# Kernel tuning notes

Hardware: AMD Instinct MI355X
Metric: run time of the kernel (lower is better)

Reference implementation:

```python
import jax, jax.numpy as jnp
import numpy as np

B, L, D, H, E, K = 16, 197, 768, 12, 8, 2
HID = 4 * D
HD = D // H
SCALE = HD ** -0.5
EPS = 1e-5


def _layernorm(x, g, b):
    m = jnp.mean(x, axis=-1, keepdims=True)
    v = jnp.mean((x - m) ** 2, axis=-1, keepdims=True)
    return (x - m) * jax.lax.rsqrt(v + EPS) * g + b


def setup_inputs() -> dict:
    key = jax.random.key(0)
    ks = jax.random.split(key, 8)
    s = 0.02
    return {
        "x": jax.random.normal(ks[0], (B, L, D), jnp.float32),
        "ln1_g": jnp.ones((D,), jnp.float32),
        "ln1_b": jnp.zeros((D,), jnp.float32),
        "qkv_w": jax.random.normal(ks[1], (D, 3 * D), jnp.float32) * s,
        "qkv_b": jnp.zeros((3 * D,), jnp.float32),
        "proj_w": jax.random.normal(ks[2], (D, D), jnp.float32) * s,
        "proj_b": jnp.zeros((D,), jnp.float32),
        "ln2_g": jnp.ones((D,), jnp.float32),
        "ln2_b": jnp.zeros((D,), jnp.float32),
        "w_gate": jax.random.normal(ks[3], (D, E), jnp.float32) * s,
        "w1": jax.random.normal(ks[4], (E, D, HID), jnp.float32) * s,
        "b1": jnp.zeros((E, HID), jnp.float32),
        "w2": jax.random.normal(ks[5], (E, HID, D), jnp.float32) * s,
        "b2": jnp.zeros((E, D), jnp.float32),
    }


def reference(x, ln1_g, ln1_b, qkv_w, qkv_b, proj_w, proj_b,
              ln2_g, ln2_b, w_gate, w1, b1, w2, b2):
    # --- attention branch: x = x + attn(norm1(x)) ---
    h = _layernorm(x, ln1_g, ln1_b)
    qkv = (h @ qkv_w + qkv_b).reshape(B, L, 3, H, HD)
    q, k, v = [qkv[:, :, i].transpose(0, 2, 1, 3) for i in range(3)]  # [B,H,L,HD]
    attn = jax.nn.softmax(jnp.einsum('bhqd,bhkd->bhqk', q, k) * SCALE, axis=-1)
    o = jnp.einsum('bhqk,bhkd->bhqd', attn, v).transpose(0, 2, 1, 3).reshape(B, L, D)
    x = x + o @ proj_w + proj_b

    # --- MoE FFN branch on norm2(x), tokens flattened ---
    flat = _layernorm(x, ln2_g, ln2_b).reshape(-1, D)  # [T, D], T = B*L
    T = flat.shape[0]
    # noisy top-k gating, eval path (no noise): top-(k+1) logits, softmax over top-k
    logits = flat @ w_gate                              # [T, E]
    top_vals, top_idx = jax.lax.top_k(logits, K + 1)
    probs = jax.nn.softmax(top_vals[:, :K], axis=-1)    # [T, K]
    gates = jnp.zeros((T, E), flat.dtype).at[
        jnp.arange(T)[:, None], top_idx[:, :K]].set(probs)  # sparse gate matrix

    # dense equivalent of SparseDispatcher dispatch -> expert MLP -> combine:
    # output[t] = sum_e gates[t,e] * (gelu(flat @ w1[e] + b1[e]) @ w2[e] + b2[e])
    hid = jax.nn.gelu(jnp.einsum('td,edf->tef', flat, w1) + b1, approximate=False)
    y = jnp.einsum('te,tef,efd->td', gates, hid, w2) + gates @ b2
    return x + y.reshape(B, L, D)
```

## Files before the change

kernel.cpp:

```cpp
#include <hip/hip_runtime.h>
#include <math.h>
#include <stdint.h>

typedef unsigned short u16;
typedef unsigned int u32;
typedef float floatx4 __attribute__((ext_vector_type(4)));
typedef __bf16 bf16x8 __attribute__((ext_vector_type(8)));

#define T_TOK 3152
#define SEQ 197
#define NH 12
#define LISTN 7424
#define MOE_MT 58

__device__ __forceinline__ float bf2f(u16 u) { return __uint_as_float(((u32)u) << 16); }
__device__ __forceinline__ u16 f2bf(float f) {
    u32 u = __float_as_uint(f);
    u += 0x7FFFu + ((u >> 16) & 1u);
    return (u16)(u >> 16);
}
__device__ __forceinline__ float wred_sum(float v) {
#pragma unroll
    for (int off = 32; off; off >>= 1) v += __shfl_xor(v, off);
    return v;
}
__device__ __forceinline__ int wred_sum_i(int v) {
#pragma unroll
    for (int off = 32; off; off >>= 1) v += __shfl_xor(v, off);
    return v;
}

__device__ __forceinline__ float gelu_fast(float v) {
    float x = fabsf(v) * 0.70710678118654752f;
    float t = __builtin_amdgcn_rcpf(fmaf(0.3275911f, x, 1.0f));
    float p = t * fmaf(t, fmaf(t, fmaf(t, fmaf(t, 1.061405429f, -1.453152027f),
                                       1.421413741f), -0.284496736f), 0.254829592f);
    float er = fmaf(-p, __expf(-x * x), 1.0f);
    er = copysignf(er, v);
    return 0.5f * v * (1.0f + er);
}

#define GLB_AS(p) ((const __attribute__((address_space(1))) void*)(uintptr_t)(p))
#define LDS_AS(p) ((__attribute__((address_space(3))) void*)(uintptr_t)(p))
__device__ __forceinline__ void gl_lds16(const u16* g, u16* l) {
    __builtin_amdgcn_global_load_lds(GLB_AS(g), LDS_AS(l), 16, 0, 0);
}

__device__ __forceinline__ void transp_tile(const float* __restrict__ in,
        u16* __restrict__ oh, u16* __restrict__ ol, int R, int C,
        int rt, int ct, int z, bool split, float (*Lt)[68]) {
    int r0 = rt * 64, c0 = ct * 64;
    size_t zo = (size_t)z * R * C;
    int tid = threadIdx.x;
    int rr = tid >> 2, cs = (tid & 3) * 16;
    const float* src = in + zo + (size_t)(r0 + rr) * C + c0 + cs;
#pragma unroll
    for (int i = 0; i < 4; i++) *(float4*)&Lt[rr][cs + i * 4] = *(const float4*)(src + i * 4);
    __syncthreads();
    int cw = tid >> 2, rs = (tid & 3) * 16;
    u16 hv[16], lv[16];
#pragma unroll
    for (int j2 = 0; j2 < 16; j2++) {
        float v = Lt[rs + j2][cw];
        u16 hb = f2bf(v);
        hv[j2] = hb;
        if (split) lv[j2] = f2bf(v - bf2f(hb));
    }
    u16* dst = oh + zo + (size_t)(c0 + cw) * R + r0 + rs;
    *(uint4*)dst = *(const uint4*)&hv[0];
    *(uint4*)(dst + 8) = *(const uint4*)&hv[8];
    if (split) {
        u16* dstl = ol + zo + (size_t)(c0 + cw) * R + r0 + rs;
        *(uint4*)dstl = *(const uint4*)&lv[0];
        *(uint4*)(dstl + 8) = *(const uint4*)&lv[8];
    }
}

#define PREP_QKVT 432
#define PREP_PROJT 144
#define PREP_W1T 4608
#define PREP_W2T 4608
#define PREP_TOTAL (PREP_QKVT + PREP_PROJT + PREP_W1T + PREP_W2T + 1)

__global__ __launch_bounds__(256) void prep_kernel(
        const float* __restrict__ qkv_w, u16* __restrict__ qkvt_h, u16* __restrict__ qkvt_l,
        const float* __restrict__ proj_w, u16* __restrict__ projt_h, u16* __restrict__ projt_l,
        const float* __restrict__ w1, u16* __restrict__ w1t,
        const float* __restrict__ w2, u16* __restrict__ w2t,
        const float* __restrict__ wg, float* __restrict__ wgT) {
    __shared__ float Lt[64][68];
    int bid = blockIdx.x;
    if (bid < PREP_QKVT) {
        transp_tile(qkv_w, qkvt_h, qkvt_l, 768, 2304, bid % 12, bid / 12, 0, true, Lt);
    } else if (bid < PREP_QKVT + PREP_PROJT) {
        int lb = bid - PREP_QKVT;
        transp_tile(proj_w, projt_h, projt_l, 768, 768, lb % 12, lb / 12, 0, true, Lt);
    } else if (bid < PREP_QKVT + PREP_PROJT + PREP_W1T) {
        int lb = bid - (PREP_QKVT + PREP_PROJT);
        int z = lb / (12 * 48), rem = lb % (12 * 48);
        transp_tile(w1, w1t, nullptr, 768, 3072, rem % 12, rem / 12, z, false, Lt);
    } else if (bid < PREP_QKVT + PREP_PROJT + PREP_W1T + PREP_W2T) {
        int lb = bid - (PREP_QKVT + PREP_PROJT + PREP_W1T);
        int z = lb / (48 * 12), rem = lb % (48 * 12);
        transp_tile(w2, w2t, nullptr, 3072, 768, rem % 48, rem / 48, z, false, Lt);
    } else {
        for (int i = threadIdx.x; i < 768 * 8; i += 256) {
            int d2 = i >> 3, e = i & 7;
            wgT[e * 768 + d2] = wg[i];
        }
    }
}

__global__ __launch_bounds__(256) void ln1_kernel(const float* __restrict__ x,
        const float* __restrict__ g, const float* __restrict__ b,
        u16* __restrict__ h_hi, u16* __restrict__ h_lo) {
    int t = blockIdx.x, tid = threadIdx.x;
    int w = tid >> 6, lane = tid & 63;
    float v[3];
#pragma unroll
    for (int i = 0; i < 3; i++) v[i] = x[(size_t)t * 768 + tid + i * 256];
    float s = v[0] + v[1] + v[2];
    float q = v[0] * v[0] + v[1] * v[1] + v[2] * v[2];
    s = wred_sum(s); q = wred_sum(q);
    __shared__ float red[8];
    if (lane == 0) { red[w] = s; red[4 + w] = q; }
    __syncthreads();
    float st = red[0] + red[1] + red[2] + red[3];
    float qt = red[4] + red[5] + red[6] + red[7];
    float mean = st * (1.f / 768.f);
    float var = qt * (1.f / 768.f) - mean * mean;
    float rs = rsqrtf(var + 1e-5f);
#pragma unroll
    for (int i = 0; i < 3; i++) {
        int d = tid + i * 256;
        float hv = (v[i] - mean) * rs * g[d] + b[d];
        u16 hi = f2bf(hv);
        h_hi[(size_t)t * 768 + d] = hi;
        h_lo[(size_t)t * 768 + d] = f2bf(hv - bf2f(hi));
    }
}

template <int MODE>
__global__ __launch_bounds__(256) void gemm128(const u16* __restrict__ Ah,
        const u16* __restrict__ Al, const u16* __restrict__ Bh, const u16* __restrict__ Bl,
        const float* __restrict__ bias, void* __restrict__ Cv, void* __restrict__ Cv2,
        const float* __restrict__ resid,
        const int* __restrict__ list, const int* __restrict__ asg, int M, int N, int K) {
    constexpr bool SPLIT = (MODE <= 1);
    constexpr int GX = (MODE <= 1) ? 25 : MOE_MT;
    constexpr int GY = (MODE == 0) ? 18 : (MODE == 2) ? 24 : 6;
    constexpr int GZ = (MODE == 3) ? 2 : 1;
    constexpr int G  = GX * GY * GZ;
    constexpr int NT = GY * GZ;
    constexpr int Q8 = G >> 3, R8 = G & 7;

    int d = blockIdx.x + GX * (blockIdx.y + GY * blockIdx.z);
    int j = d & 7, s = d >> 3;
    int v = (j < R8) ? (j * (Q8 + 1) + s) : (R8 * (Q8 + 1) + (j - R8) * Q8 + s);
    int mt = v / NT, nzr = v - mt * NT;
    int yt = nzr % GY, zt = nzr / GY;
    int m0 = mt * 128, n0 = yt * 128;

    const u16* Bph = Bh;
    const float* bp = bias;
    const u16* Bpl = Bl;
    if (MODE >= 2) {
        if (m0 >= asg[8]) return;
        int e = 0;
        while (m0 >= asg[e + 1]) ++e;
        Bph = Bh + (size_t)e * N * K;
        bp = bias + (size_t)e * N;
    }
    int kbeg = 0, kend = K;
    if (MODE == 3) { int kh = K >> 1; kbeg = zt * kh; kend = kbeg + kh; }

    __shared__ __align__(16) u16 SM[SPLIT ? 32768 : 24576];
    u16* Ash = SM;
    u16* Bsh = SM + (SPLIT ? 8192 : 12288);
    u16* Asl = SM + 16384;
    u16* Bsl = SM + 24576;

    int tid = threadIdx.x;
    int w = tid >> 6, lane = tid & 63, l15 = lane & 15, quad = lane >> 4;
    int wm = (w & 1) * 64, wn = (w >> 1) * 64;
    int lr = lane >> 2;
    int lc = ((lane & 3) ^ ((lane >> 3) & 3)) * 8;

    const u16* ga[2]; const u16* gal[2];
    const u16* gb[2]; const u16* gbl[2];
    int ldro[2];
#pragma unroll
    for (int it = 0; it < 2; it++) {
        int arow = m0 + it * 64 + w * 16 + lr;
        if (MODE == 2) {
            int entry = list[arow];
            ga[it] = Ah + (size_t)(entry >= 0 ? (entry >> 1) : 0) * K + lc;
        } else if (MODE == 3) {
            ga[it] = Ah + (size_t)arow * K + lc;
        } else {
            int rc = min(arow, M - 1);
            ga[it] = Ah + (size_t)rc * K + lc;
            gal[it] = Al + (size_t)rc * K + lc;
        }
        int brow = n0 + it * 64 + w * 16 + lr;
        gb[it] = Bph + (size_t)brow * K + lc;
        if (SPLIT) gbl[it] = Bpl + (size_t)brow * K + lc;
        ldro[it] = (it * 64 + w * 16) * 32;
    }

    int ra[4], rb[4];
#pragma unroll
    for (int i = 0; i < 4; i++) {
        int r1 = wm + i * 16 + l15;
        ra[i] = r1 * 32 + (quad ^ ((r1 >> 1) & 3)) * 8;
        int r2 = wn + i * 16 + l15;
        rb[i] = r2 * 32 + (quad ^ ((r2 >> 1) & 3)) * 8;
    }

    floatx4 acc[4][4];
#pragma unroll
    for (int mi = 0; mi < 4; mi++)
#pragma unroll
        for (int ni = 0; ni < 4; ni++) acc[mi][ni] = (floatx4){0.f, 0.f, 0.f, 0.f};

    auto stage = [&](int buf, int k0) {
        int bo = buf * 4096;
#pragma unroll
        for (int it = 0; it < 2; it++) {
            gl_lds16(ga[it] + k0, &Ash[bo + ldro[it]]);
            gl_lds16(gb[it] + k0, &Bsh[bo + ldro[it]]);
            if constexpr (SPLIT) {
                gl_lds16(gal[it] + k0, &Asl[bo + ldro[it]]);
                gl_lds16(gbl[it] + k0, &Bsl[bo + ldro[it]]);
            }
        }
    };
    auto compute = [&](int buf) {
        int bo = buf * 4096;
        bf16x8 afh[4], bfh[4], afl[4], bfl[4];
#pragma unroll
        for (int i = 0; i < 4; i++) {
            afh[i] = *(const bf16x8*)&Ash[bo + ra[i]];
            bfh[i] = *(const bf16x8*)&Bsh[bo + rb[i]];
            if constexpr (SPLIT) {
                afl[i] = *(const bf16x8*)&Asl[bo + ra[i]];
                bfl[i] = *(const bf16x8*)&Bsl[bo + rb[i]];
            }
        }
        __builtin_amdgcn_s_setprio(1);
#pragma unroll
        for (int mi = 0; mi < 4; mi++)
#pragma unroll
            for (int ni = 0; ni < 4; ni++) {
                if constexpr (SPLIT) {
                    acc[mi][ni] = __builtin_amdgcn_mfma_f32_16x16x32_bf16(afl[mi], bfh[ni], acc[mi][ni], 0, 0, 0);
                    acc[mi][ni] = __builtin_amdgcn_mfma_f32_16x16x32_bf16(afh[mi], bfl[ni], acc[mi][ni], 0, 0, 0);
                }
                acc[mi][ni] = __builtin_amdgcn_mfma_f32_16x16x32_bf16(afh[mi], bfh[ni], acc[mi][ni], 0, 0, 0);
            }
        __builtin_amdgcn_s_setprio(0);
    };

    int nsteps = (kend - kbeg) >> 5;
    if constexpr (SPLIT) {
        stage(0, kbeg);
        stage(1, kbeg + 32);
        asm volatile("s_waitcnt vmcnt(8)" ::: "memory");
        __builtin_amdgcn_s_barrier();
        for (int t = 0; t < nsteps; ++t) {
            compute(t & 1);
            asm volatile("s_waitcnt lgkmcnt(0)" ::: "memory");
            if (t + 1 < nsteps)
                asm volatile("s_waitcnt vmcnt(0)" ::: "memory");
            __builtin_amdgcn_s_barrier();
            if (t + 2 < nsteps) stage(t & 1, kbeg + (t + 2) * 32);
        }
    } else {
        stage(0, kbeg);
        stage(1, kbeg + 32);
        asm volatile("s_waitcnt vmcnt(4)" ::: "memory");
        __builtin_amdgcn_s_barrier();
        int bufc = 0;
        for (int t = 0; t < nsteps; ++t) {
            int b2 = bufc + 2; if (b2 >= 3) b2 -= 3;
            if (t + 2 < nsteps) stage(b2, kbeg + (t + 2) * 32);
            compute(bufc);
            if (t + 2 < nsteps) {
                asm volatile("s_waitcnt vmcnt(4) lgkmcnt(0)" ::: "memory");
            } else {
                asm volatile("s_waitcnt vmcnt(0) lgkmcnt(0)" ::: "memory");
            }
            __builtin_amdgcn_s_barrier();
            bufc = (bufc == 2) ? 0 : bufc + 1;
        }
    }

    if constexpr (MODE == 2) {
#pragma unroll
        for (int ni = 0; ni < 4; ni++) {
            int col = wn + ni * 16 + l15;
            float bb = bp[n0 + col];
#pragma unroll
            for (int mi = 0; mi < 4; mi++) {
#pragma unroll
                for (int r = 0; r < 4; r++) {
                    int row = wm + mi * 16 + quad * 4 + r;
                    float gv = gelu_fast(acc[mi][ni][r] + bb);
                    SM[row * 128 + (col ^ ((row & 7) << 3))] = f2bf(gv);
                }
            }
        }
        __syncthreads();
        int rr = tid >> 1, half = (tid & 1) * 64;
        int grow = m0 + rr;
        if (list[grow] >= 0) {
            u16* dst = (u16*)Cv + (size_t)grow * N + n0 + half;
            int xr = (rr & 7) << 3;
#pragma unroll
            for (int gch = 0; gch < 8; gch++) {
                int cb = (half + gch * 8) ^ xr;
                *(uint4*)(dst + gch * 8) = *(const uint4*)&SM[rr * 128 + cb];
            }
        }
        return;
    }

    float* Cf = (float*)Cv;
    if (MODE == 3 && zt != 0) Cf = (float*)Cv2;
#pragma unroll
    for (int ni = 0; ni < 4; ni++) {
        int col = n0 + wn + ni * 16 + l15;
        float bb = bp[col];
        if (MODE == 3 && zt != 0) bb = 0.f;
#pragma unroll
        for (int mi = 0; mi < 4; mi++) {
#pragma unroll
            for (int r = 0; r < 4; r++) {
                int row = m0 + wm + mi * 16 + quad * 4 + r;
                float v2 = acc[mi][ni][r] + bb;
                if (MODE == 0) {
                    if (row < M) {
                        u16 hb = f2bf(v2);
                        ((u16*)Cv)[(size_t)row * N + col] = hb;
                        ((u16*)Cv2)[(size_t)row * N + col] = f2bf(v2 - bf2f(hb));
                    }
                } else if (MODE == 1) {
                    if (row < M) Cf[(size_t)row * N + col] = v2 + resid[(size_t)row * N + col];
                } else {
                    if (list[row] >= 0) Cf[(size_t)row * N + col] = v2;
                }
            }
        }
    }
}

__global__ __launch_bounds__(256) void attn_mfma_kernel(const u16* __restrict__ qph,
        const u16* __restrict__ qpl, u16* __restrict__ ohi, u16* __restrict__ olo) {
    int d = blockIdx.x + 4 * blockIdx.y;
    int j = d & 7, sdx = d >> 3;
    int v = j * 96 + sdx;
    int qbase = (v & 3) * 64;
    int by = v >> 2;
    int b = by / NH, h = by % NH;
    int tid = threadIdx.x;
    int w = tid >> 6, lane = tid & 63, l15 = lane & 15, quad = lane >> 4;

    __shared__ u16 Qh[64 * 64], Ql[64 * 64];
    __shared__ u16 Sh[64 * 64], Sl[64 * 64];
    __shared__ u16 Ph[64 * 72], Pl[64 * 72];

    int grow8 = lane >> 3;
    int gsrc = ((lane & 7) ^ grow8) * 8;
    int srow = tid >> 2;
    int scol = (tid & 3) * 16;

#pragma unroll
    for (int it = 0; it < 2; it++) {
        int r = qbase + w * 16 + it * 8 + grow8;
        int rc = min(r, SEQ - 1);
        size_t so = (size_t)(b * SEQ + rc) * 2304 + h * 64 + gsrc;
        gl_lds16(qph + so, &Qh[(w * 16 + it * 8) * 64]);
        gl_lds16(qpl + so, &Ql[(w * 16 + it * 8) * 64]);
    }
    __syncthreads();
    bf16x8 aqh[2], aql[2];
#pragma unroll
    for (int s2 = 0; s2 < 2; s2++) {
        int row = w * 16 + l15;
        int ad = row * 64 + (((s2 * 4 + quad) ^ (row & 7))) * 8;
        aqh[s2] = *(const bf16x8*)&Qh[ad];
        aql[s2] = *(const bf16x8*)&Ql[ad];
    }

    floatx4 sc[16];
#pragma unroll
    for (int f = 0; f < 16; f++) sc[f] = (floatx4){0.f, 0.f, 0.f, 0.f};

    for (int t = 0; t < 4; t++) {
#pragma unroll
        for (int it = 0; it < 2; it++) {
            int r = t * 64 + w * 16 + it * 8 + grow8;
            int rc = min(r, SEQ - 1);
            size_t so = (size_t)(b * SEQ + rc) * 2304 + 768 + h * 64 + gsrc;
            gl_lds16(qph + so, &Sh[(w * 16 + it * 8) * 64]);
            gl_lds16(qpl + so, &Sl[(w * 16 + it * 8) * 64]);
        }
        __syncthreads();
#pragma unroll
        for (int s = 0; s < 4; s++) {
            int row = s * 16 + l15;
#pragma unroll
            for (int s2 = 0; s2 < 2; s2++) {
                int ad = row * 64 + (((s2 * 4 + quad) ^ (row & 7))) * 8;
                bf16x8 bkh = *(const bf16x8*)&Sh[ad];
                bf16x8 bkl = *(const bf16x8*)&Sl[ad];
                sc[t * 4 + s] = __builtin_amdgcn_mfma_f32_16x16x32_bf16(aql[s2], bkh, sc[t * 4 + s], 0, 0, 0);
                sc[t * 4 + s] = __builtin_amdgcn_mfma_f32_16x16x32_bf16(aqh[s2], bkl, sc[t * 4 + s], 0, 0, 0);
                sc[t * 4 + s] = __builtin_amdgcn_mfma_f32_16x16x32_bf16(aqh[s2], bkh, sc[t * 4 + s], 0, 0, 0);
            }
        }
        __syncthreads();
    }

    float m[4] = {-1e30f, -1e30f, -1e30f, -1e30f};
#pragma unroll
    for (int f = 0; f < 16; f++) {
        int key = (f >> 2) * 64 + (f & 3) * 16 + l15;
        bool valid = key < SEQ;
#pragma unroll
        for (int r = 0; r < 4; r++) {
            float s = valid ? sc[f][r] * 0.125f : -1e30f;
            sc[f][r] = s;
            m[r] = fmaxf(m[r], s);
        }
    }
#pragma unroll
    for (int r = 0; r < 4; r++) {
#pragma unroll
        for (int off = 1; off < 16; off <<= 1) m[r] = fmaxf(m[r], __shfl_xor(m[r], off));
    }
    float sum[4] = {0.f, 0.f, 0.f, 0.f};
#pragma unroll
    for (int f = 0; f < 16; f++) {
#pragma unroll
        for (int r = 0; r < 4; r++) {
            float p = expf(sc[f][r] - m[r]);
            sc[f][r] = p;
            sum[r] += p;
        }
    }
    float inv[4];
#pragma unroll
    for (int r = 0; r < 4; r++) {
#pragma unroll
        for (int off = 1; off < 16; off <<= 1) sum[r] += __shfl_xor(sum[r], off);
        inv[r] = 1.f / sum[r];
    }

    floatx4 oacc[4];
#pragma unroll
    for (int sd = 0; sd < 4; sd++) oacc[sd] = (floatx4){0.f, 0.f, 0.f, 0.f};

    for (int t = 0; t < 4; t++) {
#pragma unroll
        for (int s = 0; s < 4; s++) {
#pragma unroll
            for (int r = 0; r < 4; r++) {
                float p = sc[t * 4 + s][r];
                u16 hb = f2bf(p);
                int row = w * 16 + quad * 4 + r;
                Ph[row * 72 + s * 16 + l15] = hb;
                Pl[row * 72 + s * 16 + l15] = f2bf(p - bf2f(hb));
            }
        }
        {
            int key = t * 64 + srow;
            int kc = min(key, SEQ - 1);
            size_t so = (size_t)(b * SEQ + kc) * 2304 + 1536 + h * 64 + scol;
            u16 hv[16], lv[16];
            *(uint4*)&hv[0] = *(const uint4*)(qph + so);
            *(uint4*)&hv[8] = *(const uint4*)(qph + so + 8);
            *(uint4*)&lv[0] = *(const uint4*)(qpl + so);
            *(uint4*)&lv[8] = *(const uint4*)(qpl + so + 8);
            int kg = srow >> 3, kw = srow & 7;
#pragma unroll
            for (int i = 0; i < 16; i++) {
                int dcol = scol + i;
                int idx2 = dcol * 64 + ((kg ^ (dcol & 7)) * 8) + kw;
                Sh[idx2] = hv[i];
                Sl[idx2] = lv[i];
            }
        }
        __syncthreads();
#pragma unroll
        for (int s2 = 0; s2 < 2; s2++) {
            bf16x8 aph = *(const bf16x8*)&Ph[(w * 16 + l15) * 72 + s2 * 32 + quad * 8];
            bf16x8 apl = *(const bf16x8*)&Pl[(w * 16 + l15) * 72 + s2 * 32 + quad * 8];
#pragma unroll
            for (int sd = 0; sd < 4; sd++) {
                int row = sd * 16 + l15;
                int ad = row * 64 + (((s2 * 4 + quad) ^ (row & 7))) * 8;
                bf16x8 bvh = *(const bf16x8*)&Sh[ad];
                bf16x8 bvl = *(const bf16x8*)&Sl[ad];
                oacc[sd] = __builtin_amdgcn_mfma_f32_16x16x32_bf16(apl, bvh, oacc[sd], 0, 0, 0);
                oacc[sd] = __builtin_amdgcn_mfma_f32_16x16x32_bf16(aph, bvl, oacc[sd], 0, 0, 0);
                oacc[sd] = __builtin_amdgcn_mfma_f32_16x16x32_bf16(aph, bvh, oacc[sd], 0, 0, 0);
            }
        }
        __syncthreads();
    }

#pragma unroll
    for (int sd = 0; sd < 4; sd++) {
#pragma unroll
        for (int r = 0; r < 4; r++) {
            int q = qbase + w * 16 + quad * 4 + r;
            if (q < SEQ) {
                float val = oacc[sd][r] * inv[r];
                u16 hb = f2bf(val);
                size_t o = ((size_t)(b * SEQ + q)) * 768 + h * 64 + sd * 16 + l15;
                ohi[o] = hb;
                olo[o] = f2bf(val - bf2f(hb));
            }
        }
    }
}

__global__ __launch_bounds__(256) void ln2_gate_kernel(const float* __restrict__ x1,
        const float* __restrict__ g, const float* __restrict__ b, const float* __restrict__ wgT,
        u16* __restrict__ flat, int2* __restrict__ idx, float2* __restrict__ gate) {
    int w = threadIdx.x >> 6, lane = threadIdx.x & 63;
    int t = blockIdx.x * 4 + w;
    if (t >= T_TOK) return;
    const float* xp = x1 + (size_t)t * 768;
    float v[3][4];
    float s = 0.f, q = 0.f;
#pragma unroll
    for (int i = 0; i < 3; i++) {
        float4 f4 = *(const float4*)(xp + i * 256 + lane * 4);
        v[i][0] = f4.x; v[i][1] = f4.y; v[i][2] = f4.z; v[i][3] = f4.w;
#pragma unroll
        for (int j2 = 0; j2 < 4; j2++) { s += v[i][j2]; q += v[i][j2] * v[i][j2]; }
    }
    s = wred_sum(s); q = wred_sum(q);
    float mean = s * (1.f / 768.f);
    float var = q * (1.f / 768.f) - mean * mean;
    float rs = rsqrtf(var + 1e-5f);
    float fs[3][4];
#pragma unroll
    for (int i = 0; i < 3; i++) {
        int d0 = i * 256 + lane * 4;
        float4 g4 = *(const float4*)(g + d0);
        float4 b4 = *(const float4*)(b + d0);
        float gg[4] = {g4.x, g4.y, g4.z, g4.w};
        float bb[4] = {b4.x, b4.y, b4.z, b4.w};
        u16 hv[4];
#pragma unroll
        for (int j2 = 0; j2 < 4; j2++) {
            float f = (v[i][j2] - mean) * rs * gg[j2] + bb[j2];
            fs[i][j2] = f;
            hv[j2] = f2bf(f);
        }
        *(uint2*)&flat[(size_t)t * 768 + d0] = *(const uint2*)hv;
    }
    float lg[8];
#pragma unroll
    for (int e = 0; e < 8; e++) {
        float p = 0.f;
#pragma unroll
        for (int i = 0; i < 3; i++) {
            float4 wv = *(const float4*)(wgT + e * 768 + i * 256 + lane * 4);
            p = fmaf(fs[i][0], wv.x, p);
            p = fmaf(fs[i][1], wv.y, p);
            p = fmaf(fs[i][2], wv.z, p);
            p = fmaf(fs[i][3], wv.w, p);
        }
        lg[e] = wred_sum(p);
    }
    if (lane == 0) {
        float b0 = -1e30f, b1 = -1e30f;
        int i0 = 0, i1 = 0;
#pragma unroll
        for (int e = 0; e < 8; e++) {
            float le = lg[e];
            if (le > b0) { b1 = b0; i1 = i0; b0 = le; i0 = e; }
            else if (le > b1) { b1 = le; i1 = e; }
        }
        float ex = expf(b1 - b0);
        float den = 1.f + ex;
        idx[t] = make_int2(i0, i1);
        gate[t] = make_float2(1.f / den, ex / den);
    }
}

__global__ __launch_bounds__(256) void route_kernel(const int2* __restrict__ idx,
        int* __restrict__ asg, int* __restrict__ list, int* __restrict__ pos) {
    int tid = threadIdx.x, w = tid >> 6, lane = tid & 63;
    __shared__ int wcnt[4][8];
    __shared__ int run[8];

    int myc[8] = {0, 0, 0, 0, 0, 0, 0, 0};
    for (int t = tid; t < T_TOK; t += 256) {
        int2 id = idx[t];
#pragma unroll
        for (int e = 0; e < 8; e++) myc[e] += (id.x == e) + (id.y == e);
    }
#pragma unroll
    for (int e = 0; e < 8; e++) {
        int c = wred_sum_i(myc[e]);
        if (lane == 0) wcnt[w][e] = c;
    }
    __syncthreads();
    if (tid == 0) {
        int acc = 0;
        for (int e = 0; e < 8; e++) {
            run[e] = acc;
            asg[e] = acc;
            int c = wcnt[0][e] + wcnt[1][e] + wcnt[2][e] + wcnt[3][e];
            acc += (c + 127) & ~127;
        }
        asg[8] = acc;
    }
    __syncthreads();

    unsigned long long lt = (1ull << lane) - 1ull;
    for (int c0 = 0; c0 < T_TOK; c0 += 256) {
        int t = c0 + tid;
        bool valid = t < T_TOK;
        int ex = valid ? idx[t].x : -1;
        int ey = valid ? idx[t].y : -1;
        int rkx = 0, rky = 0;
        int wtot[8];
#pragma unroll
        for (int e = 0; e < 8; e++) {
            unsigned long long mx = __ballot(ex == e);
            unsigned long long my = __ballot(ey == e);
            int r = __popcll(mx & lt) + __popcll(my & lt);
            if (ex == e) rkx = r;
            if (ey == e) rky = r;
            wtot[e] = __popcll(mx) + __popcll(my);
        }
        if (lane == 0) {
#pragma unroll
            for (int e = 0; e < 8; e++) wcnt[w][e] = wtot[e];
        }
        __syncthreads();
        if (valid) {
            int wpx = 0, wpy = 0;
            for (int w2 = 0; w2 < w; w2++) { wpx += wcnt[w2][ex]; wpy += wcnt[w2][ey]; }
            int p0 = run[ex] + wpx + rkx;
            int p1 = run[ey] + wpy + rky;
            list[p0] = t * 2;
            pos[t * 2] = p0;
            list[p1] = t * 2 + 1;
            pos[t * 2 + 1] = p1;
        }
        __syncthreads();
        if (tid < 8) run[tid] += wcnt[0][tid] + wcnt[1][tid] + wcnt[2][tid] + wcnt[3][tid];
        __syncthreads();
    }
}

__global__ __launch_bounds__(256) void final_kernel(const float* __restrict__ x1,
        const float* __restrict__ yp0, const float* __restrict__ yp1, const int* __restrict__ pos,
        const float2* __restrict__ gate, float* __restrict__ out) {
    int t = blockIdx.x, tid = threadIdx.x;
    float2 g = gate[t];
    int p0 = pos[t * 2], p1 = pos[t * 2 + 1];
#pragma unroll
    for (int i = 0; i < 3; i++) {
        int d = tid + i * 256;
        float y0 = yp0[(size_t)p0 * 768 + d] + yp1[(size_t)p0 * 768 + d];
        float y1 = yp0[(size_t)p1 * 768 + d] + yp1[(size_t)p1 * 768 + d];
        out[(size_t)t * 768 + d] = x1[(size_t)t * 768 + d] + g.x * y0 + g.y * y1;
    }
}

extern "C" void kernel_launch(void* const* d_in, const int* in_sizes, int n_in,
                              void* d_out, int out_size, void* d_ws, size_t ws_size,
                              hipStream_t stream) {
    const float* x      = (const float*)d_in[0];
    const float* ln1_g  = (const float*)d_in[1];
    const float* ln1_b  = (const float*)d_in[2];
    const float* qkv_w  = (const float*)d_in[3];
    const float* qkv_b  = (const float*)d_in[4];
    const float* proj_w = (const float*)d_in[5];
    const float* proj_b = (const float*)d_in[6];
    const float* ln2_g  = (const float*)d_in[7];
    const float* ln2_b  = (const float*)d_in[8];
    const float* w_gate = (const float*)d_in[9];
    const float* w1     = (const float*)d_in[10];
    const float* b1     = (const float*)d_in[11];
    const float* w2     = (const float*)d_in[12];
    const float* b2     = (const float*)d_in[13];

    char* ws = (char*)d_ws;
    size_t off = 0;
    auto alloc = [&](size_t bytes) { size_t cur = off; off = (off + bytes + 255) & ~(size_t)255; return cur; };
    u16*    h_hi   = (u16*)   (ws + alloc((size_t)T_TOK * 768 * 2));
    u16*    h_lo   = (u16*)   (ws + alloc((size_t)T_TOK * 768 * 2));
    u16*    qkv_hi = (u16*)   (ws + alloc((size_t)T_TOK * 2304 * 2));
    u16*    qkv_lo = (u16*)   (ws + alloc((size_t)T_TOK * 2304 * 2));
    u16*    o_hi   = (u16*)   (ws + alloc((size_t)T_TOK * 768 * 2));
    u16*    o_lo   = (u16*)   (ws + alloc((size_t)T_TOK * 768 * 2));
    float*  ypair0 = (float*) ws;
    float*  x1     = (float*) (ws + alloc((size_t)T_TOK * 768 * 4));
    u16*    flat   = (u16*)   (ws + alloc((size_t)T_TOK * 768 * 2));
    int2*   idx    = (int2*)  (ws + alloc((size_t)T_TOK * 8));
    float2* gate   = (float2*)(ws + alloc((size_t)T_TOK * 8));
    float*  wgT    = (float*) (ws + alloc((size_t)8 * 768 * 4));
    int*    asg    = (int*)   (ws + alloc(64));
    int*    list   = (int*)   (ws + alloc((size_t)LISTN * 4));
    int*    pos    = (int*)   (ws + alloc((size_t)T_TOK * 2 * 4));
    u16*    hid    = (u16*)   (ws + alloc((size_t)LISTN * 3072 * 2));
    u16*    qkvt_h = (u16*)   (ws + alloc((size_t)2304 * 768 * 2));
    u16*    qkvt_l = (u16*)   (ws + alloc((size_t)2304 * 768 * 2));
    u16*    projt_h = (u16*)  (ws + alloc((size_t)768 * 768 * 2));
    u16*    projt_l = (u16*)  (ws + alloc((size_t)768 * 768 * 2));
    u16*    w1t    = (u16*)   (ws + alloc((size_t)8 * 3072 * 768 * 2));
    u16*    w2t    = (u16*)   (ws + alloc((size_t)8 * 768 * 3072 * 2));
    float*  ypair1 = (float*) w1t;

    hipMemsetAsync(list, 0xFF, (size_t)LISTN * 4, stream);

    prep_kernel<<<PREP_TOTAL, 256, 0, stream>>>(qkv_w, qkvt_h, qkvt_l, proj_w, projt_h, projt_l,
                                                w1, w1t, w2, w2t, w_gate, wgT);

    ln1_kernel<<<T_TOK, 256, 0, stream>>>(x, ln1_g, ln1_b, h_hi, h_lo);
    gemm128<0><<<dim3(25, 18), 256, 0, stream>>>(h_hi, h_lo, qkvt_h, qkvt_l, qkv_b, qkv_hi,
                                                 qkv_lo, nullptr, nullptr, nullptr, T_TOK, 2304, 768);
    attn_mfma_kernel<<<dim3(4, 192), 256, 0, stream>>>(qkv_hi, qkv_lo, o_hi, o_lo);
    gemm128<1><<<dim3(25, 6), 256, 0, stream>>>(o_hi, o_lo, projt_h, projt_l, proj_b, x1,
                                                nullptr, x, nullptr, nullptr, T_TOK, 768, 768);
    ln2_gate_kernel<<<T_TOK / 4, 256, 0, stream>>>(x1, ln2_g, ln2_b, wgT, flat, idx, gate);
    route_kernel<<<1, 256, 0, stream>>>(idx, asg, list, pos);
    gemm128<2><<<dim3(MOE_MT, 24), 256, 0, stream>>>(flat, nullptr, w1t, nullptr, b1, hid,
                                                     nullptr, nullptr, list, asg, LISTN, 3072, 768);
    gemm128<3><<<dim3(MOE_MT, 6, 2), 256, 0, stream>>>(hid, nullptr, w2t, nullptr, b2, ypair0,
                                                       ypair1, nullptr, list, asg, LISTN, 768, 3072);
    final_kernel<<<T_TOK, 256, 0, stream>>>(x1, ypair0, ypair1, pos, gate, (float*)d_out);
}
```

Measured before the change: 489.5 us.

## Fuse LN1 into prep kernel, swizzle transpose LDS, double-buffer W2 GEMM

Folds the LN1 normalization into the weight-prep kernel as extra blocks, removing one kernel launch. Adds an XOR swizzle to the transpose tile's LDS writes and reads to cut bank conflicts on the column-wise read. Switches the MODE 3 expert down-projection GEMM from the triple-buffered pipeline to the double-buffered path with a smaller shared footprint, which may raise occupancy but exposes more load latency.

```diff
diff --git a/kernel.cpp b/kernel.cpp
--- a/kernel.cpp
+++ b/kernel.cpp
@@ -53,15 +53,22 @@
     size_t zo = (size_t)z * R * C;
     int tid = threadIdx.x;
     int rr = tid >> 2, cs = (tid & 3) * 16;
+    int ksw = ((rr >> 4) & 3) << 1;
     const float* src = in + zo + (size_t)(r0 + rr) * C + c0 + cs;
 #pragma unroll
-    for (int i = 0; i < 4; i++) *(float4*)&Lt[rr][cs + i * 4] = *(const float4*)(src + i * 4);
+    for (int i = 0; i < 4; i++) {
+        int pq = ((cs >> 2) + i) ^ ksw;
+        *(float4*)&Lt[rr][pq * 4] = *(const float4*)(src + i * 4);
+    }
     __syncthreads();
     int cw = tid >> 2, rs = (tid & 3) * 16;
+    int cq = cw >> 2, cm = cw & 3;
     u16 hv[16], lv[16];
 #pragma unroll
     for (int j2 = 0; j2 < 16; j2++) {
-        float v = Lt[rs + j2][cw];
+        int row = rs + j2;
+        int pq = cq ^ (((row >> 4) & 3) << 1);
+        float v = Lt[row][pq * 4 + cm];
         u16 hb = f2bf(v);
         hv[j2] = hb;
         if (split) lv[j2] = f2bf(v - bf2f(hb));
@@ -80,14 +87,17 @@
 #define PREP_PROJT 144
 #define PREP_W1T 4608
 #define PREP_W2T 4608
-#define PREP_TOTAL (PREP_QKVT + PREP_PROJT + PREP_W1T + PREP_W2T + 1)
+#define PREP_WG (PREP_QKVT + PREP_PROJT + PREP_W1T + PREP_W2T)
+#define PREP_TOTAL (PREP_WG + 1 + T_TOK)
 
 __global__ __launch_bounds__(256) void prep_kernel(
         const float* __restrict__ qkv_w, u16* __restrict__ qkvt_h, u16* __restrict__ qkvt_l,
         const float* __restrict__ proj_w, u16* __restrict__ projt_h, u16* __restrict__ projt_l,
         const float* __restrict__ w1, u16* __restrict__ w1t,
         const float* __restrict__ w2, u16* __restrict__ w2t,
-        const float* __restrict__ wg, float* __restrict__ wgT) {
+        const float* __restrict__ wg, float* __restrict__ wgT,
+        const float* __restrict__ x, const float* __restrict__ ln1_g,
+        const float* __restrict__ ln1_b, u16* __restrict__ h_hi, u16* __restrict__ h_lo) {
     __shared__ float Lt[64][68];
     int bid = blockIdx.x;
     if (bid < PREP_QKVT) {
@@ -99,44 +109,40 @@
         int lb = bid - (PREP_QKVT + PREP_PROJT);
         int z = lb / (12 * 48), rem = lb % (12 * 48);
         transp_tile(w1, w1t, nullptr, 768, 3072, rem % 12, rem / 12, z, false, Lt);
-    } else if (bid < PREP_QKVT + PREP_PROJT + PREP_W1T + PREP_W2T) {
+    } else if (bid < PREP_WG) {
         int lb = bid - (PREP_QKVT + PREP_PROJT + PREP_W1T);
         int z = lb / (48 * 12), rem = lb % (48 * 12);
         transp_tile(w2, w2t, nullptr, 3072, 768, rem % 48, rem / 48, z, false, Lt);
-    } else {
+    } else if (bid == PREP_WG) {
         for (int i = threadIdx.x; i < 768 * 8; i += 256) {
             int d2 = i >> 3, e = i & 7;
             wgT[e * 768 + d2] = wg[i];
         }
-    }
-}
-
-__global__ __launch_bounds__(256) void ln1_kernel(const float* __restrict__ x,
-        const float* __restrict__ g, const float* __restrict__ b,
-        u16* __restrict__ h_hi, u16* __restrict__ h_lo) {
-    int t = blockIdx.x, tid = threadIdx.x;
-    int w = tid >> 6, lane = tid & 63;
-    float v[3];
-#pragma unroll
-    for (int i = 0; i < 3; i++) v[i] = x[(size_t)t * 768 + tid + i * 256];
-    float s = v[0] + v[1] + v[2];
-    float q = v[0] * v[0] + v[1] * v[1] + v[2] * v[2];
-    s = wred_sum(s); q = wred_sum(q);
-    __shared__ float red[8];
-    if (lane == 0) { red[w] = s; red[4 + w] = q; }
-    __syncthreads();
-    float st = red[0] + red[1] + red[2] + red[3];
-    float qt = red[4] + red[5] + red[6] + red[7];
-    float mean = st * (1.f / 768.f);
-    float var = qt * (1.f / 768.f) - mean * mean;
-    float rs = rsqrtf(var + 1e-5f);
-#pragma unroll
-    for (int i = 0; i < 3; i++) {
-        int d = tid + i * 256;
-        float hv = (v[i] - mean) * rs * g[d] + b[d];
-        u16 hi = f2bf(hv);
-        h_hi[(size_t)t * 768 + d] = hi;
-        h_lo[(size_t)t * 768 + d] = f2bf(hv - bf2f(hi));
+    } else {
+        int t = bid - (PREP_WG + 1), tid = threadIdx.x;
+        int w = tid >> 6, lane = tid & 63;
+        float* red = &Lt[0][0];
+        float v[3];
+#pragma unroll
+        for (int i = 0; i < 3; i++) v[i] = x[(size_t)t * 768 + tid + i * 256];
+        float s = v[0] + v[1] + v[2];
+        float q = v[0] * v[0] + v[1] * v[1] + v[2] * v[2];
+        s = wred_sum(s); q = wred_sum(q);
+        if (lane == 0) { red[w] = s; red[4 + w] = q; }
+        __syncthreads();
+        float st = red[0] + red[1] + red[2] + red[3];
+        float qt = red[4] + red[5] + red[6] + red[7];
+        float mean = st * (1.f / 768.f);
+        float var = qt * (1.f / 768.f) - mean * mean;
+        float rs = rsqrtf(var + 1e-5f);
+#pragma unroll
+        for (int i = 0; i < 3; i++) {
+            int d = tid + i * 256;
+            float hv = (v[i] - mean) * rs * ln1_g[d] + ln1_b[d];
+            u16 hi = f2bf(hv);
+            h_hi[(size_t)t * 768 + d] = hi;
+            h_lo[(size_t)t * 768 + d] = f2bf(hv - bf2f(hi));
+        }
     }
 }
 
@@ -174,9 +180,9 @@
     int kbeg = 0, kend = K;
     if (MODE == 3) { int kh = K >> 1; kbeg = zt * kh; kend = kbeg + kh; }
 
-    __shared__ __align__(16) u16 SM[SPLIT ? 32768 : 24576];
+    __shared__ __align__(16) u16 SM[SPLIT ? 32768 : (MODE == 2 ? 24576 : 16384)];
     u16* Ash = SM;
-    u16* Bsh = SM + (SPLIT ? 8192 : 12288);
+    u16* Bsh = SM + (MODE == 2 ? 12288 : 8192);
     u16* Asl = SM + 16384;
     u16* Bsl = SM + 24576;
 
@@ -262,10 +268,11 @@
     };
 
     int nsteps = (kend - kbeg) >> 5;
-    if constexpr (SPLIT) {
+    if constexpr (MODE != 2) {
         stage(0, kbeg);
         stage(1, kbeg + 32);
-        asm volatile("s_waitcnt vmcnt(8)" ::: "memory");
+        if constexpr (SPLIT) asm volatile("s_waitcnt vmcnt(8)" ::: "memory");
+        else                 asm volatile("s_waitcnt vmcnt(4)" ::: "memory");
         __builtin_amdgcn_s_barrier();
         for (int t = 0; t < nsteps; ++t) {
             compute(t & 1);
@@ -724,9 +731,9 @@
     hipMemsetAsync(list, 0xFF, (size_t)LISTN * 4, stream);
 
     prep_kernel<<<PREP_TOTAL, 256, 0, stream>>>(qkv_w, qkvt_h, qkvt_l, proj_w, projt_h, projt_l,
-                                                w1, w1t, w2, w2t, w_gate, wgT);
-
-    ln1_kernel<<<T_TOK, 256, 0, stream>>>(x, ln1_g, ln1_b, h_hi, h_lo);
+                                                w1, w1t, w2, w2t, w_gate, wgT,
+                                                x, ln1_g, ln1_b, h_hi, h_lo);
+
     gemm128<0><<<dim3(25, 18), 256, 0, stream>>>(h_hi, h_lo, qkvt_h, qkvt_l, qkv_b, qkv_hi,
                                                  qkv_lo, nullptr, nullptr, nullptr, T_TOK, 2304, 768);
     attn_mfma_kernel<<<dim3(4, 192), 256, 0, stream>>>(qkv_hi, qkv_lo, o_hi, o_lo);
```

New measurement: 504.9 us. 1.03x slower.
